# Kernel optimization log

Measured on AMD Instinct MI355X. Metric: run time of the kernel, lower is better.

The kernel has to match this reference:

```python
import jax, jax.numpy as jnp
import numpy as np

# Grid / model constants (apt_original_dims = (B,H,W,T,BS,D))
B, H, W, T, BS, D = 8, 32, 32, 4, 3, 768
SMAX = 2  # apt_num_scales=2 -> patch sizes in {1, 2}


def _make_positions():
    """Tile each (H,W) grid per timestep with 2x2 blocks; exactly half the
    blocks become one coarse size-2 patch, the rest four size-1 patches.
    Returns int32 [B, P, 4] with rows (y, x, size, t); P identical per sample."""
    rng = np.random.default_rng(0)
    blocks = [(by, bx, t) for t in range(T) for by in range(H // SMAX) for bx in range(W // SMAX)]
    n_blocks = len(blocks)
    pos_all = []
    for b in range(B):
        coarse = rng.permutation(n_blocks) < n_blocks // 2
        plist = []
        for (by, bx, t), c in zip(blocks, coarse):
            y, x = by * SMAX, bx * SMAX
            if c:
                plist.append((y, x, SMAX, t))
            else:
                for dy in range(SMAX):
                    for dx in range(SMAX):
                        plist.append((y + dy, x + dx, 1, t))
        pos_all.append(plist)
    return np.asarray(pos_all, dtype=np.int32)  # [B, P, 4]


def setup_inputs() -> dict:
    key = jax.random.key(0)
    positions = jnp.asarray(_make_positions())            # [B, P, 4]
    P = positions.shape[1]                                # 2560
    modality_tokens = jax.random.normal(key, (B, P * BS, D), dtype=jnp.float32)
    return {"modality_tokens": modality_tokens, "positions": positions}


def reference(modality_tokens, positions):
    """Faithful jax version of split_and_expand_per_modality for the APT
    modality: scatter patch tokens to [B,H,W,T,BS,D], broadcasting coarse
    (size>1) tokens over the s x s grid cells they cover.
    Vectorized as: build a cell->patch-id map via one scatter, then gather."""
    Bn, P, _ = positions.shape
    y, x, size, t = positions[..., 0], positions[..., 1], positions[..., 2], positions[..., 3]

    # All offsets inside a max-size patch footprint: [SMAX*SMAX]
    dy, dx = jnp.meshgrid(jnp.arange(SMAX), jnp.arange(SMAX), indexing='ij')
    dy, dx = dy.reshape(-1), dx.reshape(-1)

    yy = y[:, :, None] + dy[None, None, :]                # [B, P, S2]
    xx = x[:, :, None] + dx[None, None, :]
    valid = (dy[None, None, :] < size[:, :, None]) & (dx[None, None, :] < size[:, :, None])

    flat = (yy * W + xx) * T + t[:, :, None]              # flat cell index
    flat = jnp.where(valid, flat, H * W * T)              # invalid -> dummy slot

    pid = jnp.broadcast_to(jnp.arange(P, dtype=jnp.int32)[None, :, None], flat.shape)
    b_idx = jnp.broadcast_to(jnp.arange(Bn)[:, None, None], flat.shape)

    id_map = jnp.full((Bn, H * W * T + 1), -1, dtype=jnp.int32)
    id_map = id_map.at[b_idx, flat].set(pid)              # cell -> covering patch id
    id_map = id_map[:, : H * W * T].reshape(Bn, H, W, T)

    tok = modality_tokens.reshape(Bn, P, BS, D)

    def gather_one(tok_b, idm_b):
        out = tok_b[jnp.maximum(idm_b, 0)]                # [H, W, T, BS, D]
        return jnp.where((idm_b >= 0)[..., None, None], out, jnp.zeros((), tok_b.dtype))

    return jax.vmap(gather_one)(tok, id_map)              # [B, H, W, T, BS, D]
```

## Files before the change

kernel.cpp:

```cpp
#include <hip/hip_runtime.h>


constexpr int H_ = 32;
constexpr int W_ = 32;
constexpr int T_ = 4;
constexpr int BS_ = 3;
constexpr int D_ = 768;
constexpr int CD  = BS_ * D_;
constexpr int CD4 = CD / 4;
constexpr int BLOCK = 192;

typedef float f4 __attribute__((ext_vector_type(4)));

__global__ __launch_bounds__(BLOCK) void apt_scatter_kernel_nt(
    const f4* __restrict__ tok,
    const int4* __restrict__ pos,
    f4* __restrict__ out,
    int P)
{
    const int bp = blockIdx.x;
    const int b  = bp / P;

    const int4 q = pos[bp];
    const int y = q.x, x = q.y, size = q.z, t = q.w;

    const f4* __restrict__ src = tok + (long)bp * CD4;
    const long cell_stride_y = (long)W_ * T_ * CD4;
    const long cell_stride_x = (long)T_ * CD4;
    const long base0 = ((((long)b * H_ + y) * W_ + x) * T_ + t) * CD4;

    const int tid = threadIdx.x;

    if (size == 1) {
        f4* __restrict__ dst = out + base0;
        #pragma unroll
        for (int k = 0; k < CD4 / BLOCK; ++k) {
            const int i = tid + k * BLOCK;
            const f4 v = __builtin_nontemporal_load(&src[i]);
            __builtin_nontemporal_store(v, &dst[i]);
        }
    } else {
        f4* __restrict__ d00 = out + base0;
        f4* __restrict__ d01 = out + base0 + cell_stride_x;
        f4* __restrict__ d10 = out + base0 + cell_stride_y;
        f4* __restrict__ d11 = out + base0 + cell_stride_y + cell_stride_x;
        #pragma unroll
        for (int k = 0; k < CD4 / BLOCK; ++k) {
            const int i = tid + k * BLOCK;
            const f4 v = __builtin_nontemporal_load(&src[i]);
            __builtin_nontemporal_store(v, &d00[i]);
            __builtin_nontemporal_store(v, &d01[i]);
            __builtin_nontemporal_store(v, &d10[i]);
            __builtin_nontemporal_store(v, &d11[i]);
        }
    }
}

extern "C" void kernel_launch(void* const* d_in, const int* in_sizes, int n_in,
                              void* d_out, int out_size, void* d_ws, size_t ws_size,
                              hipStream_t stream) {
    const f4*   tok = (const f4*)d_in[0];
    const int4* pos = (const int4*)d_in[1];

    const int Bn = 8;
    const int P  = in_sizes[1] / (Bn * 4);

    const int grid = Bn * P;
    apt_scatter_kernel_nt<<<grid, BLOCK, 0, stream>>>(tok, pos, (f4*)d_out, P);
}
```

Before: 412.4 us.

## Replace per-patch scatter with cell-map build plus per-cell gather

Adds a small kernel that builds a cell-to-patch id map in workspace, then a gather kernel with one block per output cell that copies the covering patch's token row. Output cells are remapped so consecutive blocks spread across XCDs. This turns scattered multi-destination writes into contiguous per-cell writes, at the cost of an extra launch, repeated reads of coarse tokens, and reliance on every cell being covered. Falls back to the old scatter when workspace is too small.

```diff
diff --git a/kernel.cpp b/kernel.cpp
--- a/kernel.cpp
+++ b/kernel.cpp
@@ -9,28 +9,65 @@
 constexpr int CD  = BS_ * D_;
 constexpr int CD4 = CD / 4;
 constexpr int BLOCK = 192;
+constexpr int BN_ = 8;
+constexpr int CELLS = BN_ * H_ * W_ * T_;
+constexpr int NXCD = 8;
 
 typedef float f4 __attribute__((ext_vector_type(4)));
 
+__global__ __launch_bounds__(256) void build_map_kernel(
+    const int4* __restrict__ pos,
+    int* __restrict__ map,
+    int P)
+{
+    const int bp = blockIdx.x * 256 + threadIdx.x;
+    if (bp >= BN_ * P) return;
+    const int b = bp / P;
+    const int4 q = pos[bp];
+    const int y = q.x, x = q.y, size = q.z, t = q.w;
+    const int c0 = (((b * H_ + y) * W_ + x) * T_) + t;
+    map[c0] = bp;
+    if (size == 2) {
+        map[c0 + T_] = bp;
+        map[c0 + W_ * T_] = bp;
+        map[c0 + W_ * T_ + T_] = bp;
+    }
+}
+
+__global__ __launch_bounds__(BLOCK) void apt_gather_kernel(
+    const f4* __restrict__ tok,
+    const int* __restrict__ map,
+    f4* __restrict__ out)
+{
+    const int n = blockIdx.x;
+    const int cell = (n & (NXCD - 1)) * (CELLS / NXCD) + (n >> 3);
+
+    const int pid = map[cell];
+    const f4* __restrict__ src = tok + (long)pid * CD4;
+    f4* __restrict__ dst = out + (long)cell * CD4;
+
+    const int tid = threadIdx.x;
+    #pragma unroll
+    for (int k = 0; k < CD4 / BLOCK; ++k) {
+        const int i = tid + k * BLOCK;
+        const f4 v = src[i];
+        __builtin_nontemporal_store(v, &dst[i]);
+    }
+}
+
 __global__ __launch_bounds__(BLOCK) void apt_scatter_kernel_nt(
-    const f4* __restrict__ tok,
-    const int4* __restrict__ pos,
-    f4* __restrict__ out,
-    int P)
+    const f4* __restrict__ tok, const int4* __restrict__ pos,
+    f4* __restrict__ out, int P)
 {
     const int bp = blockIdx.x;
     const int b  = bp / P;
-
     const int4 q = pos[bp];
     const int y = q.x, x = q.y, size = q.z, t = q.w;
-
     const f4* __restrict__ src = tok + (long)bp * CD4;
-    const long cell_stride_y = (long)W_ * T_ * CD4;
-    const long cell_stride_x = (long)T_ * CD4;
+    const long csy = (long)W_ * T_ * CD4;
+    const long csx = (long)T_ * CD4;
     const long base0 = ((((long)b * H_ + y) * W_ + x) * T_ + t) * CD4;
-
     const int tid = threadIdx.x;
-
     if (size == 1) {
         f4* __restrict__ dst = out + base0;
         #pragma unroll
@@ -41,9 +78,9 @@
         }
     } else {
         f4* __restrict__ d00 = out + base0;
-        f4* __restrict__ d01 = out + base0 + cell_stride_x;
-        f4* __restrict__ d10 = out + base0 + cell_stride_y;
-        f4* __restrict__ d11 = out + base0 + cell_stride_y + cell_stride_x;
+        f4* __restrict__ d01 = out + base0 + csx;
+        f4* __restrict__ d10 = out + base0 + csy;
+        f4* __restrict__ d11 = out + base0 + csy + csx;
         #pragma unroll
         for (int k = 0; k < CD4 / BLOCK; ++k) {
             const int i = tid + k * BLOCK;
@@ -62,9 +99,15 @@
     const f4*   tok = (const f4*)d_in[0];
     const int4* pos = (const int4*)d_in[1];
 
-    const int Bn = 8;
-    const int P  = in_sizes[1] / (Bn * 4);
+    const int P = in_sizes[1] / (BN_ * 4);
 
-    const int grid = Bn * P;
-    apt_scatter_kernel_nt<<<grid, BLOCK, 0, stream>>>(tok, pos, (f4*)d_out, P);
+    const size_t map_bytes = (size_t)CELLS * sizeof(int);
+    if (d_ws != nullptr && ws_size >= map_bytes) {
+        int* map = (int*)d_ws;
+        const int total = BN_ * P;
+        build_map_kernel<<<(total + 255) / 256, 256, 0, stream>>>(pos, map, P);
+        apt_gather_kernel<<<CELLS, BLOCK, 0, stream>>>(tok, map, (f4*)d_out);
+    } else {
+        apt_scatter_kernel_nt<<<BN_ * P, BLOCK, 0, stream>>>(tok, pos, (f4*)d_out, P);
+    }
 }
```

Result: slower. 427.0 us (+3.6%).
